# Kernel optimization log

Hardware: AMD Instinct MI355X
Metric: run time of the kernel (lower is better)

The kernel has to match this reference:

```python
import jax, jax.numpy as jnp
import numpy as np

B, S, H = 4, 1024, 1024
N, D = 16, 64  # num_heads, head_dim (key_dim = value_dim = H // N)
FF = 4096
EPS = 1e-5


def _glorot(key, shape):
    fan_in, fan_out = shape[-2], shape[-1]
    lim = np.sqrt(6.0 / (fan_in + fan_out))
    return jax.random.uniform(key, shape, jnp.float32, -lim, lim)


def setup_inputs() -> dict:
    key = jax.random.key(0)
    ks = jax.random.split(key, 32)
    inp = {
        "x": jax.random.normal(ks[0], (B, S, H), jnp.float32),
        # per-head complex Q/K projections (ComplexDense = two real Dense layers)
        "Wq_r": _glorot(ks[1], (N, H, D)), "Wq_i": _glorot(ks[2], (N, H, D)),
        "bq_r": jnp.zeros((N, D)), "bq_i": jnp.zeros((N, D)),
        "Wk_r": _glorot(ks[3], (N, H, D)), "Wk_i": _glorot(ks[4], (N, H, D)),
        "bk_r": jnp.zeros((N, D)), "bk_i": jnp.zeros((N, D)),
        # per-head real value projection
        "Wv": _glorot(ks[5], (N, H, D)), "bv": jnp.zeros((N, D)),
        # per-head positional interference weights (seq_len, key_dim)
        "pos_q_r": _glorot(ks[6], (N, S, D)), "pos_q_i": _glorot(ks[7], (N, S, D)),
        "pos_k_r": _glorot(ks[8], (N, S, D)), "pos_k_i": _glorot(ks[9], (N, S, D)),
        # multi-head output projection
        "Wo": _glorot(ks[10], (H, H)), "bo": jnp.zeros((H,)),
        # feedforward
        "W1": _glorot(ks[11], (H, FF)), "b1": jnp.zeros((FF,)),
        "W2": _glorot(ks[12], (FF, H)), "b2": jnp.zeros((H,)),
        # layer norms
        "g1": jnp.ones((H,)), "beta1": jnp.zeros((H,)),
        "g2": jnp.ones((H,)), "beta2": jnp.zeros((H,)),
    }
    return inp


def _layer_norm(x, g, b):
    mu = jnp.mean(x, axis=-1, keepdims=True)
    var = jnp.mean(jnp.square(x - mu), axis=-1, keepdims=True)
    return (x - mu) * jax.lax.rsqrt(var + EPS) * g + b


def reference(x, Wq_r, Wq_i, bq_r, bq_i, Wk_r, Wk_i, bk_r, bk_i, Wv, bv,
              pos_q_r, pos_q_i, pos_k_r, pos_k_i, Wo, bo, W1, b1, W2, b2,
              g1, beta1, g2, beta2):
    scale = 1.0 / np.sqrt(float(D))  # applied twice, as in the original
    # complex Q/K projections, all heads at once: [B,N,S,D]
    qr = jnp.einsum('bsh,nhd->bnsd', x, Wq_r) + bq_r[:, None, :]
    qi = jnp.einsum('bsh,nhd->bnsd', x, Wq_i) + bq_i[:, None, :]
    kr = jnp.einsum('bsh,nhd->bnsd', x, Wk_r) + bk_r[:, None, :]
    ki = jnp.einsum('bsh,nhd->bnsd', x, Wk_i) + bk_i[:, None, :]
    v = jnp.einsum('bsh,nhd->bnsd', x, Wv) + bv[:, None, :]
    # query scaled by 1/sqrt(D), then positional interference added (query and key)
    qr = qr * scale + pos_q_r[None]
    qi = qi * scale + pos_q_i[None]
    kr = kr + pos_k_r[None]
    ki = ki + pos_k_i[None]
    # real part of complex matmul q @ k^T (transpose_b, no conjugation), rescaled
    scores = (jnp.einsum('bnsd,bntd->bnst', qr, kr)
              - jnp.einsum('bnsd,bntd->bnst', qi, ki)) * scale
    probs = jax.nn.softmax(scores, axis=-1)  # temperature == 1.0 (use_temperature=False)
    heads = jnp.einsum('bnst,bntd->bnsd', probs, v)
    concat = heads.transpose(0, 2, 1, 3).reshape(x.shape[0], x.shape[1], N * D)
    attn_out = concat @ Wo + bo
    h1 = _layer_norm(x + attn_out, g1, beta1)
    ff = jax.nn.relu(h1 @ W1 + b1) @ W2 + b2
    return _layer_norm(h1 + ff, g2, beta2)
```

## Files before the change

### kernel.cpp

```cpp
#include <hip/hip_runtime.h>
#include <math.h>

typedef unsigned short u16;
typedef unsigned int   u32;
typedef __attribute__((ext_vector_type(8))) short short8;
typedef __attribute__((ext_vector_type(4))) float f32x4;
typedef __attribute__((ext_vector_type(4))) u16   us4;

constexpr int Bc = 4, Sc = 1024, Hc = 1024, Nc = 16, Dc = 64, FFc = 4096;

__device__ __forceinline__ u16 bfh(float v) {
  u32 u = __float_as_uint(v);
  return (u16)((u + 0x7FFFu + ((u >> 16) & 1u)) >> 16);
}
__device__ __forceinline__ void split2(float v, u16& h, u16& l) {
  h = bfh(v);
  l = bfh(v - __uint_as_float(((u32)h) << 16));
}

__device__ __forceinline__ void gl_lds16(const u16* g, u16* lds) {
  __builtin_amdgcn_global_load_lds(
      (const __attribute__((address_space(1))) void*)g,
      (__attribute__((address_space(3))) void*)lds, 16, 0, 0);
}

__device__ __forceinline__ f32x4 mfma_bf16(short8 a, short8 b, f32x4 c) {
  asm("v_mfma_f32_16x16x32_bf16 %0, %1, %2, %0" : "+v"(c) : "v"(a), "v"(b));
  return c;
}

__global__ __launch_bounds__(256)
void split_copy(const float* __restrict__ in, u16* __restrict__ oh,
                u16* __restrict__ ol, int n4) {
  int i = blockIdx.x * 256 + threadIdx.x;
  if (i >= n4) return;
  f32x4 v = ((const f32x4*)in)[i];
  us4 h4, l4;
#pragma unroll
  for (int c = 0; c < 4; ++c) { u16 h, l; split2(v[c], h, l); h4[c] = h; l4[c] = l; }
  ((us4*)oh)[i] = h4;
  ((us4*)ol)[i] = l4;
}

__global__ __launch_bounds__(256)
void transpose_split(const float* __restrict__ in, u16* __restrict__ oh,
                     u16* __restrict__ ol, int R, int C) {
  __shared__ float t[32][33];
  const int c0 = blockIdx.x * 32, r0 = blockIdx.y * 32;
  const int tx = threadIdx.x & 31, ty = threadIdx.x >> 5;
#pragma unroll
  for (int j = 0; j < 4; ++j)
    t[ty + 8 * j][tx] = in[(size_t)(r0 + ty + 8 * j) * C + c0 + tx];
  __syncthreads();
#pragma unroll
  for (int j = 0; j < 4; ++j) {
    float v = t[tx][ty + 8 * j];
    u16 h, l; split2(v, h, l);
    size_t o = (size_t)(c0 + ty + 8 * j) * R + r0 + tx;
    oh[o] = h; ol[o] = l;
  }
}

__global__ __launch_bounds__(256)
void conv_wproj(const float* __restrict__ Wqr, const float* __restrict__ Wqi,
                const float* __restrict__ Wkr, const float* __restrict__ Wki,
                const float* __restrict__ Wv,  u16* __restrict__ oh,
                u16* __restrict__ ol) {
  __shared__ float t[32][33];
  const int c0 = blockIdx.x * 32, k0 = blockIdx.y * 32;
  const int n = c0 / 320, w0 = c0 - n * 320;
  const int chunk = w0 >> 6, d0 = w0 & 63;
  const float* src; float sgn = 1.f;
  switch (chunk) {
    case 0: src = Wqr; break;
    case 1: src = Wqi; break;
    case 2: src = Wkr; break;
    case 3: src = Wki; sgn = -1.f; break;
    default: src = Wv; break;
  }
  const int tx = threadIdx.x & 31, ty = threadIdx.x >> 5;
#pragma unroll
  for (int j = 0; j < 4; ++j)
    t[ty + 8 * j][tx] = sgn * src[((size_t)n * 1024 + k0 + ty + 8 * j) * 64 + d0 + tx];
  __syncthreads();
#pragma unroll
  for (int j = 0; j < 4; ++j) {
    float v = t[tx][ty + 8 * j];
    u16 h, l; split2(v, h, l);
    size_t o = (size_t)(c0 + ty + 8 * j) * 1024 + k0 + tx;
    oh[o] = h; ol[o] = l;
  }
}

struct GemmP {
  const u16 *Ah, *Al, *Bh, *Bl;
  int N, K;
  const float* bias;
  const float* resid;
  float* outf;
  u16 *oh, *ol;
  const float *bqr, *bqi, *bkr, *bki, *bv;
  const float *pqr, *pqi, *pkr, *pki;
  u16 *qh, *ql, *kh, *kl, *vth, *vtl;
};

template<int MODE>
__global__ __launch_bounds__(256)
void mfma_gemm(GemmP p) {
  __shared__ __attribute__((aligned(16))) u16 sAh[128 * 32];
  __shared__ __attribute__((aligned(16))) u16 sAl[128 * 32];
  __shared__ __attribute__((aligned(16))) u16 sBh[128 * 32];
  __shared__ __attribute__((aligned(16))) u16 sBl[128 * 32];
  const int tid = threadIdx.x;
  const int w = tid >> 6, lane = tid & 63;
  const int wm = w >> 1, wn = w & 1;
  const int lrow = lane & 15, g = lane >> 4;
  const int bm = blockIdx.y * 128, bn = blockIdx.x * 128;
  const int K = p.K;

  const int srow = lane >> 2;
  const int sseg = (lane & 3) ^ ((lane >> 3) & 3);

  f32x4 acc[4][4];
#pragma unroll
  for (int i = 0; i < 4; ++i)
#pragma unroll
    for (int j = 0; j < 4; ++j) acc[i][j] = (f32x4){0.f, 0.f, 0.f, 0.f};

  for (int kb = 0; kb < K; kb += 32) {
#pragma unroll
    for (int i = 0; i < 2; ++i) {
      const int rowl = w * 32 + i * 16;
      const size_t ga = (size_t)(bm + rowl + srow) * K + kb + sseg * 8;
      const size_t gb = (size_t)(bn + rowl + srow) * K + kb + sseg * 8;
      const int lo = rowl * 32;
      gl_lds16(p.Ah + ga, &sAh[lo]);
      gl_lds16(p.Al + ga, &sAl[lo]);
      gl_lds16(p.Bh + gb, &sBh[lo]);
      gl_lds16(p.Bl + gb, &sBl[lo]);
    }
    __syncthreads();

    short8 ah[4], al[4], bh[4], bl[4];
    const int sw = (lrow >> 1) & 3;
#pragma unroll
    for (int mf = 0; mf < 4; ++mf) {
      int idx = (wm * 64 + mf * 16 + lrow) * 32 + ((g ^ sw) * 8);
      ah[mf] = *(const short8*)&sAh[idx];
      al[mf] = *(const short8*)&sAl[idx];
    }
#pragma unroll
    for (int nf = 0; nf < 4; ++nf) {
      int idx = (wn * 64 + nf * 16 + lrow) * 32 + ((g ^ sw) * 8);
      bh[nf] = *(const short8*)&sBh[idx];
      bl[nf] = *(const short8*)&sBl[idx];
    }
#pragma unroll
    for (int mf = 0; mf < 4; ++mf)
#pragma unroll
      for (int nf = 0; nf < 4; ++nf) {
        f32x4 a = acc[mf][nf];
        a = mfma_bf16(ah[mf], bh[nf], a);
        a = mfma_bf16(ah[mf], bl[nf], a);
        a = mfma_bf16(al[mf], bh[nf], a);
        acc[mf][nf] = a;
      }
    __syncthreads();
  }

#pragma unroll
  for (int nf = 0; nf < 4; ++nf) {
    const int c = bn + wn * 64 + nf * 16 + lrow;
    if (MODE == 0) {
      const int n = c / 320;
      const int wcol = c - n * 320;
      const int chunk = wcol >> 6, d = wcol & 63;
#pragma unroll
      for (int mf = 0; mf < 4; ++mf) {
        const int r0 = bm + wm * 64 + mf * 16 + g * 4;
        const int bb = r0 >> 10, s0 = r0 & 1023;
        const int head = bb * 16 + n;
        f32x4 a = acc[mf][nf];
        if (chunk == 4) {
          us4 hv, lv;
#pragma unroll
          for (int reg = 0; reg < 4; ++reg) {
            u16 hh, ll; split2(a[reg] + p.bv[n * 64 + d], hh, ll);
            hv[reg] = hh; lv[reg] = ll;
          }
          size_t o = ((size_t)head * 64 + d) * 1024 + s0;
          *(us4*)&p.vth[o] = hv;
          *(us4*)&p.vtl[o] = lv;
        } else {
#pragma unroll
          for (int reg = 0; reg < 4; ++reg) {
            const int s = s0 + reg;
            const size_t pidx = ((size_t)n * 1024 + s) * 64 + d;
            float val;
            u16 *dh, *dl;
            if (chunk == 0) {
              val = (a[reg] + p.bqr[n * 64 + d]) * 0.125f + p.pqr[pidx];
              dh = p.qh; dl = p.ql;
            } else if (chunk == 1) {
              val = (a[reg] + p.bqi[n * 64 + d]) * 0.125f + p.pqi[pidx];
              dh = p.qh; dl = p.ql;
            } else if (chunk == 2) {
              val = a[reg] + p.bkr[n * 64 + d] + p.pkr[pidx];
              dh = p.kh; dl = p.kl;
            } else {
              val = a[reg] - p.bki[n * 64 + d] - p.pki[pidx];
              dh = p.kh; dl = p.kl;
            }
            size_t o = ((size_t)head * 1024 + s) * 128 + (chunk & 1) * 64 + d;
            u16 hh, ll; split2(val, hh, ll);
            dh[o] = hh; dl[o] = ll;
          }
        }
      }
    } else {
      const float bb = p.bias[c];
#pragma unroll
      for (int mf = 0; mf < 4; ++mf) {
        const int r0 = bm + wm * 64 + mf * 16 + g * 4;
        f32x4 a = acc[mf][nf];
#pragma unroll
        for (int reg = 0; reg < 4; ++reg) {
          const int row = r0 + reg;
          const size_t o = (size_t)row * p.N + c;
          if (MODE == 1) {
            p.outf[o] = a[reg] + bb + p.resid[o];
          } else {
            float v = fmaxf(a[reg] + bb, 0.f);
            u16 h, l; split2(v, h, l);
            p.oh[o] = h; p.ol[o] = l;
          }
        }
      }
    }
  }
}

__global__ __launch_bounds__(256)
void attn_mfma(const u16* __restrict__ qh, const u16* __restrict__ ql,
               const u16* __restrict__ kh, const u16* __restrict__ kl,
               const u16* __restrict__ vth, const u16* __restrict__ vtl,
               u16* __restrict__ ch, u16* __restrict__ cl) {
  __shared__ __attribute__((aligned(16))) u16 ksh[64 * 128];
  __shared__ __attribute__((aligned(16))) u16 ksl[64 * 128];
  __shared__ __attribute__((aligned(16))) u16 vsh[64 * 64];
  __shared__ __attribute__((aligned(16))) u16 vsl[64 * 64];
  __shared__ __attribute__((aligned(16))) u16 ps[4][2][16 * 64];

  const int tid = threadIdx.x;
  const int w = tid >> 6, lane = tid & 63;
  const int lo16 = lane & 15, hi4 = lane >> 4;
  const int n = blockIdx.y, b = blockIdx.z;
  const int head = b * Nc + n;
  const int q0 = blockIdx.x * 64;
  const u16* qbh = qh + (size_t)head * 1024 * 128;
  const u16* qbl = ql + (size_t)head * 1024 * 128;
  const u16* kbh = kh + (size_t)head * 1024 * 128;
  const u16* kbl = kl + (size_t)head * 1024 * 128;
  const u16* vbh = vth + (size_t)head * 64 * 1024;
  const u16* vbl = vtl + (size_t)head * 64 * 1024;

  {
    const int ri = lane >> 4, slot = lane & 15;
#pragma unroll
    for (int i = 0; i < 4; ++i) {
      const int row = w * 16 + i * 4 + ri;
      const int sg = slot ^ (row & 7);
      const size_t src = (size_t)(q0 + row) * 128 + sg * 8;
      gl_lds16(qbh + src, &ksh[(w * 16 + i * 4) * 128]);
      gl_lds16(qbl + src, &ksl[(w * 16 + i * 4) * 128]);
    }
  }
  __syncthreads();
  short8 qf[2][4];
  {
    const int qrow = w * 16 + lo16;
#pragma unroll
    for (int ks = 0; ks < 4; ++ks) {
      const int addr = qrow * 128 + (((ks * 4 + hi4) ^ (qrow & 7)) * 8);
      qf[0][ks] = *(const short8*)&ksh[addr];
      qf[1][ks] = *(const short8*)&ksl[addr];
    }
  }
  __syncthreads();

  f32x4 acc_o[4];
  float m_[4], l_[4];
#pragma unroll
  for (int i = 0; i < 4; ++i) {
    acc_o[i] = (f32x4){0.f, 0.f, 0.f, 0.f};
    m_[i] = -1e30f; l_[i] = 0.f;
  }

  for (int kt = 0; kt < 16; ++kt) {
    const int k0 = kt * 64;
    {
      const int ri = lane >> 4, slot = lane & 15;
#pragma unroll
      for (int i = 0; i < 4; ++i) {
        const int row = w * 16 + i * 4 + ri;
        const int sg = slot ^ (row & 7);
        const size_t src = (size_t)(k0 + row) * 128 + sg * 8;
        gl_lds16(kbh + src, &ksh[(w * 16 + i * 4) * 128]);
        gl_lds16(kbl + src, &ksl[(w * 16 + i * 4) * 128]);
      }
      const int di = lane >> 3, vslot = lane & 7;
#pragma unroll
      for (int i = 0; i < 2; ++i) {
        const int d = w * 16 + i * 8 + di;
        const int sg = vslot ^ (d & 7);
        const size_t src = (size_t)d * 1024 + k0 + sg * 8;
        gl_lds16(vbh + src, &vsh[(w * 16 + i * 8) * 64]);
        gl_lds16(vbl + src, &vsl[(w * 16 + i * 8) * 64]);
      }
    }
    __syncthreads();

    f32x4 sc[4];
#pragma unroll
    for (int cg = 0; cg < 4; ++cg) sc[cg] = (f32x4){0.f, 0.f, 0.f, 0.f};
#pragma unroll
    for (int cg = 0; cg < 4; ++cg) {
      const int key = cg * 16 + lo16;
#pragma unroll
      for (int ks = 0; ks < 4; ++ks) {
        const int addr = key * 128 + (((ks * 4 + hi4) ^ (key & 7)) * 8);
        short8 bhf = *(const short8*)&ksh[addr];
        short8 blf = *(const short8*)&ksl[addr];
        f32x4 a = sc[cg];
        a = mfma_bf16(qf[0][ks], bhf, a);
        a = mfma_bf16(qf[0][ks], blf, a);
        a = mfma_bf16(qf[1][ks], bhf, a);
        sc[cg] = a;
      }
    }
    float pv[4][4];
#pragma unroll
    for (int reg = 0; reg < 4; ++reg) {
      float mx = fmaxf(fmaxf(sc[0][reg], sc[1][reg]),
                       fmaxf(sc[2][reg], sc[3][reg])) * 0.125f;
#pragma unroll
      for (int off = 1; off < 16; off <<= 1) mx = fmaxf(mx, __shfl_xor(mx, off));
      const float mn = fmaxf(m_[reg], mx);
      const float corr = __expf(m_[reg] - mn);
      m_[reg] = mn;
      float sum = 0.f;
#pragma unroll
      for (int cg = 0; cg < 4; ++cg) {
        float pe = __expf(sc[cg][reg] * 0.125f - mn);
        pv[cg][reg] = pe; sum += pe;
      }
#pragma unroll
      for (int off = 1; off < 16; off <<= 1) sum += __shfl_xor(sum, off);
      l_[reg] = l_[reg] * corr + sum;
#pragma unroll
      for (int cg = 0; cg < 4; ++cg) acc_o[cg][reg] *= corr;
    }
#pragma unroll
    for (int cg = 0; cg < 4; ++cg) {
      const int key = cg * 16 + lo16;
#pragma unroll
      for (int reg = 0; reg < 4; ++reg) {
        const int row = hi4 * 4 + reg;
        const int pa = row * 64 + (((key >> 3) ^ (row >> 1)) * 8) + (key & 7);
        u16 hh, ll; split2(pv[cg][reg], hh, ll);
        ps[w][0][pa] = hh;
        ps[w][1][pa] = ll;
      }
    }
    short8 pah[2], pal[2];
#pragma unroll
    for (int ks2 = 0; ks2 < 2; ++ks2) {
      const int addr = lo16 * 64 + (((ks2 * 4 + hi4) ^ (lo16 >> 1)) * 8);
      pah[ks2] = *(const short8*)&ps[w][0][addr];
      pal[ks2] = *(const short8*)&ps[w][1][addr];
    }
#pragma unroll
    for (int cg = 0; cg < 4; ++cg) {
      const int d = cg * 16 + lo16;
#pragma unroll
      for (int ks2 = 0; ks2 < 2; ++ks2) {
        const int addr = d * 64 + (((ks2 * 4 + hi4) ^ (d & 7)) * 8);
        short8 vhf = *(const short8*)&vsh[addr];
        short8 vlf = *(const short8*)&vsl[addr];
        f32x4 a = acc_o[cg];
        a = mfma_bf16(pah[ks2], vhf, a);
        a = mfma_bf16(pah[ks2], vlf, a);
        a = mfma_bf16(pal[ks2], vhf, a);
        acc_o[cg] = a;
      }
    }
    __syncthreads();
  }

  float inv[4];
#pragma unroll
  for (int reg = 0; reg < 4; ++reg) inv[reg] = 1.f / l_[reg];
#pragma unroll
  for (int cg = 0; cg < 4; ++cg) {
#pragma unroll
    for (int reg = 0; reg < 4; ++reg) {
      const int qrow = q0 + w * 16 + hi4 * 4 + reg;
      const size_t o = ((size_t)b * Sc + qrow) * 1024 + n * 64 + cg * 16 + lo16;
      u16 hh, ll; split2(acc_o[cg][reg] * inv[reg], hh, ll);
      ch[o] = hh; cl[o] = ll;
    }
  }
}

template<bool SPLIT>
__global__ __launch_bounds__(256)
void ln_kernel(const float* __restrict__ in, const float* __restrict__ gam,
               const float* __restrict__ bet, float* __restrict__ out,
               u16* __restrict__ oh, u16* __restrict__ ol) {
  const int row = blockIdx.x, t = threadIdx.x;
  f32x4 v = ((const f32x4*)(in + (size_t)row * 1024))[t];
  float s = v[0] + v[1] + v[2] + v[3];
  float q = v[0] * v[0] + v[1] * v[1] + v[2] * v[2] + v[3] * v[3];
#pragma unroll
  for (int off = 1; off < 64; off <<= 1) {
    s += __shfl_xor(s, off);
    q += __shfl_xor(q, off);
  }
  __shared__ float red[8];
  int wv = t >> 6, lnid = t & 63;
  if (lnid == 0) { red[wv] = s; red[4 + wv] = q; }
  __syncthreads();
  s = red[0] + red[1] + red[2] + red[3];
  q = red[4] + red[5] + red[6] + red[7];
  float mu = s * (1.f / 1024.f);
  float var = q * (1.f / 1024.f) - mu * mu;
  float ri = rsqrtf(var + 1e-5f);
  f32x4 g4 = ((const f32x4*)gam)[t];
  f32x4 b4 = ((const f32x4*)bet)[t];
  f32x4 o;
#pragma unroll
  for (int c = 0; c < 4; ++c) o[c] = (v[c] - mu) * ri * g4[c] + b4[c];
  ((f32x4*)(out + (size_t)row * 1024))[t] = o;
  if (SPLIT) {
    us4 h4, l4;
#pragma unroll
    for (int c = 0; c < 4; ++c) {
      u16 hh, ll; split2(o[c], hh, ll);
      h4[c] = hh; l4[c] = ll;
    }
    *(us4*)&oh[(size_t)row * 1024 + t * 4] = h4;
    *(us4*)&ol[(size_t)row * 1024 + t * 4] = l4;
  }
}

extern "C" void kernel_launch(void* const* d_in, const int* in_sizes, int n_in,
                              void* d_out, int out_size, void* d_ws, size_t ws_size,
                              hipStream_t stream) {
  const float* x    = (const float*)d_in[0];
  const float* Wq_r = (const float*)d_in[1];
  const float* Wq_i = (const float*)d_in[2];
  const float* bq_r = (const float*)d_in[3];
  const float* bq_i = (const float*)d_in[4];
  const float* Wk_r = (const float*)d_in[5];
  const float* Wk_i = (const float*)d_in[6];
  const float* bk_r = (const float*)d_in[7];
  const float* bk_i = (const float*)d_in[8];
  const float* Wv   = (const float*)d_in[9];
  const float* bv   = (const float*)d_in[10];
  const float* pq_r = (const float*)d_in[11];
  const float* pq_i = (const float*)d_in[12];
  const float* pk_r = (const float*)d_in[13];
  const float* pk_i = (const float*)d_in[14];
  const float* Wo   = (const float*)d_in[15];
  const float* bo   = (const float*)d_in[16];
  const float* W1   = (const float*)d_in[17];
  const float* b1   = (const float*)d_in[18];
  const float* W2   = (const float*)d_in[19];
  const float* b2   = (const float*)d_in[20];
  const float* g1   = (const float*)d_in[21];
  const float* be1  = (const float*)d_in[22];
  const float* g2   = (const float*)d_in[23];
  const float* be2  = (const float*)d_in[24];

  char* Wb = (char*)d_ws;
  const size_t MB = (size_t)1 << 20;
  u16* qch = (u16*)(Wb + 0 * MB);
  u16* qcl = (u16*)(Wb + 16 * MB);
  u16* kch = (u16*)(Wb + 32 * MB);
  u16* kcl = (u16*)(Wb + 48 * MB);
  u16* vth = (u16*)(Wb + 64 * MB);
  u16* vtl = (u16*)(Wb + 72 * MB);
  u16* xh  = (u16*)(Wb + 80 * MB);
  u16* xl  = (u16*)(Wb + 88 * MB);
  u16* ch  = xh; u16* cl = xl;
  u16* w2h = xh; u16* w2l = xl;
  u16* wph = (u16*)(Wb + 96 * MB);
  u16* wpl = (u16*)(Wb + 106 * MB);
  u16* w1h = (u16*)(Wb + 96 * MB);
  u16* w1l = (u16*)(Wb + 104 * MB);
  u16* woh = (u16*)(Wb + 116 * MB);
  u16* wol = (u16*)(Wb + 118 * MB);
  float* h1 = (float*)(Wb + 120 * MB);
  u16* h1h = (u16*)(Wb + 136 * MB);
  u16* h1l = (u16*)(Wb + 144 * MB);
  float* hpre = (float*)(Wb + 0 * MB);
  u16* ffh = (u16*)(Wb + 16 * MB);
  u16* ffl = (u16*)(Wb + 48 * MB);

  split_copy<<<4096, 256, 0, stream>>>(x, xh, xl, (Bc * Sc * Hc) / 4);
  conv_wproj<<<dim3(160, 32), 256, 0, stream>>>(Wq_r, Wq_i, Wk_r, Wk_i, Wv, wph, wpl);
  GemmP pp = {};
  pp.Ah = xh; pp.Al = xl; pp.Bh = wph; pp.Bl = wpl; pp.N = 5120; pp.K = 1024;
  pp.bqr = bq_r; pp.bqi = bq_i; pp.bkr = bk_r; pp.bki = bk_i; pp.bv = bv;
  pp.pqr = pq_r; pp.pqi = pq_i; pp.pkr = pk_r; pp.pki = pk_i;
  pp.qh = qch; pp.ql = qcl; pp.kh = kch; pp.kl = kcl; pp.vth = vth; pp.vtl = vtl;
  mfma_gemm<0><<<dim3(40, 32), 256, 0, stream>>>(pp);
  transpose_split<<<dim3(128, 32), 256, 0, stream>>>(W1, w1h, w1l, 1024, 4096);
  transpose_split<<<dim3(32, 32), 256, 0, stream>>>(Wo, woh, wol, 1024, 1024);
  attn_mfma<<<dim3(16, 16, 4), 256, 0, stream>>>(qch, qcl, kch, kcl, vth, vtl, ch, cl);
  GemmP po = {};
  po.Ah = ch; po.Al = cl; po.Bh = woh; po.Bl = wol; po.N = 1024; po.K = 1024;
  po.bias = bo; po.resid = x; po.outf = hpre;
  mfma_gemm<1><<<dim3(8, 32), 256, 0, stream>>>(po);
  transpose_split<<<dim3(32, 128), 256, 0, stream>>>(W2, w2h, w2l, 4096, 1024);
  ln_kernel<true><<<4096, 256, 0, stream>>>(hpre, g1, be1, h1, h1h, h1l);
  GemmP p1 = {};
  p1.Ah = h1h; p1.Al = h1l; p1.Bh = w1h; p1.Bl = w1l; p1.N = 4096; p1.K = 1024;
  p1.bias = b1; p1.oh = ffh; p1.ol = ffl;
  mfma_gemm<2><<<dim3(32, 32), 256, 0, stream>>>(p1);
  GemmP p2 = {};
  p2.Ah = ffh; p2.Al = ffl; p2.Bh = w2h; p2.Bl = w2l; p2.N = 1024; p2.K = 4096;
  p2.bias = b2; p2.resid = h1; p2.outf = hpre;
  mfma_gemm<1><<<dim3(8, 32), 256, 0, stream>>>(p2);
  ln_kernel<false><<<4096, 256, 0, stream>>>(hpre, g2, be2, (float*)d_out,
                                             nullptr, nullptr);
}
```

Baseline: 902.6 us.

## Double-buffer LDS tiles in split-bf16 MFMA GEMM to overlap loads with compute

Doubles the shared-memory staging buffers so the global-to-LDS copy of the next K slice is issued before the MFMA work on the current slice, unrolling the K loop by two. The aim is to hide global load latency that previously stalled every iteration between its load and its barrier. LDS use doubles to 64 KB per block, which may cut occupancy. The loop also assumes K is a multiple of 64.

```diff
diff --git a/kernel.cpp b/kernel.cpp
--- a/kernel.cpp
+++ b/kernel.cpp
@@ -107,10 +107,8 @@
 template<int MODE>
 __global__ __launch_bounds__(256)
 void mfma_gemm(GemmP p) {
-  __shared__ __attribute__((aligned(16))) u16 sAh[128 * 32];
-  __shared__ __attribute__((aligned(16))) u16 sAl[128 * 32];
-  __shared__ __attribute__((aligned(16))) u16 sBh[128 * 32];
-  __shared__ __attribute__((aligned(16))) u16 sBl[128 * 32];
+  __shared__ __attribute__((aligned(16))) u16 sA[2][2][128 * 32];
+  __shared__ __attribute__((aligned(16))) u16 sB[2][2][128 * 32];
   const int tid = threadIdx.x;
   const int w = tid >> 6, lane = tid & 63;
   const int wm = w >> 1, wn = w & 1;
@@ -120,6 +118,7 @@
 
   const int srow = lane >> 2;
   const int sseg = (lane & 3) ^ ((lane >> 3) & 3);
+  const int rowl0 = w * 32, rowl1 = w * 32 + 16;
 
   f32x4 acc[4][4];
 #pragma unroll
@@ -127,33 +126,35 @@
 #pragma unroll
     for (int j = 0; j < 4; ++j) acc[i][j] = (f32x4){0.f, 0.f, 0.f, 0.f};
 
-  for (int kb = 0; kb < K; kb += 32) {
-#pragma unroll
-    for (int i = 0; i < 2; ++i) {
-      const int rowl = w * 32 + i * 16;
-      const size_t ga = (size_t)(bm + rowl + srow) * K + kb + sseg * 8;
-      const size_t gb = (size_t)(bn + rowl + srow) * K + kb + sseg * 8;
-      const int lo = rowl * 32;
-      gl_lds16(p.Ah + ga, &sAh[lo]);
-      gl_lds16(p.Al + ga, &sAl[lo]);
-      gl_lds16(p.Bh + gb, &sBh[lo]);
-      gl_lds16(p.Bl + gb, &sBl[lo]);
-    }
-    __syncthreads();
-
+  auto stage = [&](int buf, int kb) {
+    const size_t ga0 = (size_t)(bm + rowl0 + srow) * K + kb + sseg * 8;
+    const size_t gb0 = (size_t)(bn + rowl0 + srow) * K + kb + sseg * 8;
+    const size_t ga1 = (size_t)(bm + rowl1 + srow) * K + kb + sseg * 8;
+    const size_t gb1 = (size_t)(bn + rowl1 + srow) * K + kb + sseg * 8;
+    gl_lds16(p.Ah + ga0, &sA[buf][0][rowl0 * 32]);
+    gl_lds16(p.Al + ga0, &sA[buf][1][rowl0 * 32]);
+    gl_lds16(p.Bh + gb0, &sB[buf][0][rowl0 * 32]);
+    gl_lds16(p.Bl + gb0, &sB[buf][1][rowl0 * 32]);
+    gl_lds16(p.Ah + ga1, &sA[buf][0][rowl1 * 32]);
+    gl_lds16(p.Al + ga1, &sA[buf][1][rowl1 * 32]);
+    gl_lds16(p.Bh + gb1, &sB[buf][0][rowl1 * 32]);
+    gl_lds16(p.Bl + gb1, &sB[buf][1][rowl1 * 32]);
+  };
+
+  const int sw = (lrow >> 1) & 3;
+  auto compute = [&](int buf) {
     short8 ah[4], al[4], bh[4], bl[4];
-    const int sw = (lrow >> 1) & 3;
 #pragma unroll
     for (int mf = 0; mf < 4; ++mf) {
       int idx = (wm * 64 + mf * 16 + lrow) * 32 + ((g ^ sw) * 8);
-      ah[mf] = *(const short8*)&sAh[idx];
-      al[mf] = *(const short8*)&sAl[idx];
+      ah[mf] = *(const short8*)&sA[buf][0][idx];
+      al[mf] = *(const short8*)&sA[buf][1][idx];
     }
 #pragma unroll
     for (int nf = 0; nf < 4; ++nf) {
       int idx = (wn * 64 + nf * 16 + lrow) * 32 + ((g ^ sw) * 8);
-      bh[nf] = *(const short8*)&sBh[idx];
-      bl[nf] = *(const short8*)&sBl[idx];
+      bh[nf] = *(const short8*)&sB[buf][0][idx];
+      bl[nf] = *(const short8*)&sB[buf][1][idx];
     }
 #pragma unroll
     for (int mf = 0; mf < 4; ++mf)
@@ -165,6 +166,16 @@
         a = mfma_bf16(al[mf], bh[nf], a);
         acc[mf][nf] = a;
       }
+  };
+
+  stage(0, 0);
+  __syncthreads();
+  for (int kb = 0; kb < K; kb += 64) {
+    stage(1, kb + 32);
+    compute(0);
+    __syncthreads();
+    if (kb + 64 < K) stage(0, kb + 64);
+    compute(1);
     __syncthreads();
   }
 
```

Result: no change. 917.6 us (+1.7%).

## Split-K the N=1024 GEMMs, fold bias/residual into LayerNorm, swizzle block order

Applied to the files above, without the earlier changes.

The output-projection and FF2 GEMMs now run with a two-way split-K (grid z=2). Each half writes raw fp32 partials to its own buffer. That doubles the block count on these narrow N=1024 GEMMs, which filled only 256 tiles before. LayerNorm is extended to sum the two partials plus bias and residual before normalising, so the GEMM epilogue no longer reads the residual. All GEMMs also remap block indices with an interleave-by-8 swizzle to change tile traversal order for cache locality. The cost is extra fp32 partial traffic (two full output-sized writes and reads) and a reshuffled workspace layout that reuses freed buffers.

```diff
diff --git a/kernel.cpp b/kernel.cpp
--- a/kernel.cpp
+++ b/kernel.cpp
@@ -94,10 +94,10 @@
 
 struct GemmP {
   const u16 *Ah, *Al, *Bh, *Bl;
-  int N, K;
+  int N, K, lda;
   const float* bias;
-  const float* resid;
   float* outf;
+  float* outf1;
   u16 *oh, *ol;
   const float *bqr, *bqi, *bkr, *bki, *bv;
   const float *pqr, *pqi, *pkr, *pki;
@@ -107,19 +107,23 @@
 template<int MODE>
 __global__ __launch_bounds__(256)
 void mfma_gemm(GemmP p) {
-  __shared__ __attribute__((aligned(16))) u16 sAh[128 * 32];
-  __shared__ __attribute__((aligned(16))) u16 sAl[128 * 32];
-  __shared__ __attribute__((aligned(16))) u16 sBh[128 * 32];
-  __shared__ __attribute__((aligned(16))) u16 sBl[128 * 32];
+  __shared__ __attribute__((aligned(16))) u16 sA[2][128 * 32];
+  __shared__ __attribute__((aligned(16))) u16 sB[2][128 * 32];
   const int tid = threadIdx.x;
   const int w = tid >> 6, lane = tid & 63;
   const int wm = w >> 1, wn = w & 1;
   const int lrow = lane & 15, g = lane >> 4;
-  const int bm = blockIdx.y * 128, bn = blockIdx.x * 128;
-  const int K = p.K;
+  const int gx = gridDim.x;
+  const int id = blockIdx.y * gx + blockIdx.x;
+  const int qq = (gx * gridDim.y) >> 3;
+  const int sid = (id & 7) * qq + (id >> 3);
+  const int bn = (sid % gx) * 128, bm = (sid / gx) * 128;
+  const int K = p.K, lda = p.lda;
+  const int koff = blockIdx.z * K;
 
   const int srow = lane >> 2;
   const int sseg = (lane & 3) ^ ((lane >> 3) & 3);
+  const int rowl0 = w * 32, rowl1 = w * 32 + 16;
 
   f32x4 acc[4][4];
 #pragma unroll
@@ -127,33 +131,34 @@
 #pragma unroll
     for (int j = 0; j < 4; ++j) acc[i][j] = (f32x4){0.f, 0.f, 0.f, 0.f};
 
+  const int sw = (lrow >> 1) & 3;
   for (int kb = 0; kb < K; kb += 32) {
-#pragma unroll
-    for (int i = 0; i < 2; ++i) {
-      const int rowl = w * 32 + i * 16;
-      const size_t ga = (size_t)(bm + rowl + srow) * K + kb + sseg * 8;
-      const size_t gb = (size_t)(bn + rowl + srow) * K + kb + sseg * 8;
-      const int lo = rowl * 32;
-      gl_lds16(p.Ah + ga, &sAh[lo]);
-      gl_lds16(p.Al + ga, &sAl[lo]);
-      gl_lds16(p.Bh + gb, &sBh[lo]);
-      gl_lds16(p.Bl + gb, &sBl[lo]);
-    }
+    const size_t ga0 = (size_t)(bm + rowl0 + srow) * lda + koff + kb + sseg * 8;
+    const size_t gb0 = (size_t)(bn + rowl0 + srow) * lda + koff + kb + sseg * 8;
+    const size_t ga1 = (size_t)(bm + rowl1 + srow) * lda + koff + kb + sseg * 8;
+    const size_t gb1 = (size_t)(bn + rowl1 + srow) * lda + koff + kb + sseg * 8;
+    gl_lds16(p.Ah + ga0, &sA[0][rowl0 * 32]);
+    gl_lds16(p.Al + ga0, &sA[1][rowl0 * 32]);
+    gl_lds16(p.Bh + gb0, &sB[0][rowl0 * 32]);
+    gl_lds16(p.Bl + gb0, &sB[1][rowl0 * 32]);
+    gl_lds16(p.Ah + ga1, &sA[0][rowl1 * 32]);
+    gl_lds16(p.Al + ga1, &sA[1][rowl1 * 32]);
+    gl_lds16(p.Bh + gb1, &sB[0][rowl1 * 32]);
+    gl_lds16(p.Bl + gb1, &sB[1][rowl1 * 32]);
     __syncthreads();
 
     short8 ah[4], al[4], bh[4], bl[4];
-    const int sw = (lrow >> 1) & 3;
 #pragma unroll
     for (int mf = 0; mf < 4; ++mf) {
       int idx = (wm * 64 + mf * 16 + lrow) * 32 + ((g ^ sw) * 8);
-      ah[mf] = *(const short8*)&sAh[idx];
-      al[mf] = *(const short8*)&sAl[idx];
+      ah[mf] = *(const short8*)&sA[0][idx];
+      al[mf] = *(const short8*)&sA[1][idx];
     }
 #pragma unroll
     for (int nf = 0; nf < 4; ++nf) {
       int idx = (wn * 64 + nf * 16 + lrow) * 32 + ((g ^ sw) * 8);
-      bh[nf] = *(const short8*)&sBh[idx];
-      bl[nf] = *(const short8*)&sBl[idx];
+      bh[nf] = *(const short8*)&sB[0][idx];
+      bl[nf] = *(const short8*)&sB[1][idx];
     }
 #pragma unroll
     for (int mf = 0; mf < 4; ++mf)
@@ -217,23 +222,28 @@
           }
         }
       }
-    } else {
-      const float bb = p.bias[c];
+    } else if (MODE == 1) {
+      float* outp = blockIdx.z ? p.outf1 : p.outf;
 #pragma unroll
       for (int mf = 0; mf < 4; ++mf) {
         const int r0 = bm + wm * 64 + mf * 16 + g * 4;
         f32x4 a = acc[mf][nf];
 #pragma unroll
+        for (int reg = 0; reg < 4; ++reg)
+          outp[(size_t)(r0 + reg) * p.N + c] = a[reg];
+      }
+    } else {
+      const float bb = p.bias[c];
+#pragma unroll
+      for (int mf = 0; mf < 4; ++mf) {
+        const int r0 = bm + wm * 64 + mf * 16 + g * 4;
+        f32x4 a = acc[mf][nf];
+#pragma unroll
         for (int reg = 0; reg < 4; ++reg) {
-          const int row = r0 + reg;
-          const size_t o = (size_t)row * p.N + c;
-          if (MODE == 1) {
-            p.outf[o] = a[reg] + bb + p.resid[o];
-          } else {
-            float v = fmaxf(a[reg] + bb, 0.f);
-            u16 h, l; split2(v, h, l);
-            p.oh[o] = h; p.ol[o] = l;
-          }
+          const size_t o = (size_t)(r0 + reg) * p.N + c;
+          float v = fmaxf(a[reg] + bb, 0.f);
+          u16 h, l; split2(v, h, l);
+          p.oh[o] = h; p.ol[o] = l;
         }
       }
     }
@@ -414,11 +424,19 @@
 
 template<bool SPLIT>
 __global__ __launch_bounds__(256)
-void ln_kernel(const float* __restrict__ in, const float* __restrict__ gam,
-               const float* __restrict__ bet, float* __restrict__ out,
-               u16* __restrict__ oh, u16* __restrict__ ol) {
+void ln_fuse(const float* __restrict__ P0, const float* __restrict__ P1,
+             const float* __restrict__ resid, const float* __restrict__ bias,
+             const float* __restrict__ gam, const float* __restrict__ bet,
+             float* __restrict__ out, u16* __restrict__ oh,
+             u16* __restrict__ ol) {
   const int row = blockIdx.x, t = threadIdx.x;
-  f32x4 v = ((const f32x4*)(in + (size_t)row * 1024))[t];
+  const size_t base = (size_t)row * 1024;
+  f32x4 v = ((const f32x4*)(P0 + base))[t];
+  f32x4 p1 = ((const f32x4*)(P1 + base))[t];
+  f32x4 rr = ((const f32x4*)(resid + base))[t];
+  f32x4 bb = ((const f32x4*)bias)[t];
+#pragma unroll
+  for (int c = 0; c < 4; ++c) v[c] += p1[c] + rr[c] + bb[c];
   float s = v[0] + v[1] + v[2] + v[3];
   float q = v[0] * v[0] + v[1] * v[1] + v[2] * v[2] + v[3] * v[3];
 #pragma unroll
@@ -440,7 +458,7 @@
   f32x4 o;
 #pragma unroll
   for (int c = 0; c < 4; ++c) o[c] = (v[c] - mu) * ri * g4[c] + b4[c];
-  ((f32x4*)(out + (size_t)row * 1024))[t] = o;
+  ((f32x4*)(out + base))[t] = o;
   if (SPLIT) {
     us4 h4, l4;
 #pragma unroll
@@ -448,8 +466,8 @@
       u16 hh, ll; split2(o[c], hh, ll);
       h4[c] = hh; l4[c] = ll;
     }
-    *(us4*)&oh[(size_t)row * 1024 + t * 4] = h4;
-    *(us4*)&ol[(size_t)row * 1024 + t * 4] = l4;
+    *(us4*)&oh[base + t * 4] = h4;
+    *(us4*)&ol[base + t * 4] = l4;
   }
 }
 
@@ -498,19 +516,23 @@
   u16* wpl = (u16*)(Wb + 106 * MB);
   u16* w1h = (u16*)(Wb + 96 * MB);
   u16* w1l = (u16*)(Wb + 104 * MB);
-  u16* woh = (u16*)(Wb + 116 * MB);
-  u16* wol = (u16*)(Wb + 118 * MB);
+  u16* woh = (u16*)(Wb + 112 * MB);
+  u16* wol = (u16*)(Wb + 114 * MB);
   float* h1 = (float*)(Wb + 120 * MB);
   u16* h1h = (u16*)(Wb + 136 * MB);
   u16* h1l = (u16*)(Wb + 144 * MB);
-  float* hpre = (float*)(Wb + 0 * MB);
-  u16* ffh = (u16*)(Wb + 16 * MB);
-  u16* ffl = (u16*)(Wb + 48 * MB);
+  float* P0 = (float*)(Wb + 0 * MB);
+  float* P1 = (float*)(Wb + 16 * MB);
+  u16* ffh = (u16*)(Wb + 0 * MB);
+  u16* ffl = (u16*)(Wb + 32 * MB);
+  float* Q0 = (float*)(Wb + 64 * MB);
+  float* Q1 = (float*)(Wb + 96 * MB);
 
   split_copy<<<4096, 256, 0, stream>>>(x, xh, xl, (Bc * Sc * Hc) / 4);
   conv_wproj<<<dim3(160, 32), 256, 0, stream>>>(Wq_r, Wq_i, Wk_r, Wk_i, Wv, wph, wpl);
   GemmP pp = {};
-  pp.Ah = xh; pp.Al = xl; pp.Bh = wph; pp.Bl = wpl; pp.N = 5120; pp.K = 1024;
+  pp.Ah = xh; pp.Al = xl; pp.Bh = wph; pp.Bl = wpl;
+  pp.N = 5120; pp.K = 1024; pp.lda = 1024;
   pp.bqr = bq_r; pp.bqi = bq_i; pp.bkr = bk_r; pp.bki = bk_i; pp.bv = bv;
   pp.pqr = pq_r; pp.pqi = pq_i; pp.pkr = pk_r; pp.pki = pk_i;
   pp.qh = qch; pp.ql = qcl; pp.kh = kch; pp.kl = kcl; pp.vth = vth; pp.vtl = vtl;
@@ -519,19 +541,22 @@
   transpose_split<<<dim3(32, 32), 256, 0, stream>>>(Wo, woh, wol, 1024, 1024);
   attn_mfma<<<dim3(16, 16, 4), 256, 0, stream>>>(qch, qcl, kch, kcl, vth, vtl, ch, cl);
   GemmP po = {};
-  po.Ah = ch; po.Al = cl; po.Bh = woh; po.Bl = wol; po.N = 1024; po.K = 1024;
-  po.bias = bo; po.resid = x; po.outf = hpre;
-  mfma_gemm<1><<<dim3(8, 32), 256, 0, stream>>>(po);
+  po.Ah = ch; po.Al = cl; po.Bh = woh; po.Bl = wol;
+  po.N = 1024; po.K = 512; po.lda = 1024;
+  po.outf = P0; po.outf1 = P1;
+  mfma_gemm<1><<<dim3(8, 32, 2), 256, 0, stream>>>(po);
   transpose_split<<<dim3(32, 128), 256, 0, stream>>>(W2, w2h, w2l, 4096, 1024);
-  ln_kernel<true><<<4096, 256, 0, stream>>>(hpre, g1, be1, h1, h1h, h1l);
+  ln_fuse<true><<<4096, 256, 0, stream>>>(P0, P1, x, bo, g1, be1, h1, h1h, h1l);
   GemmP p1 = {};
-  p1.Ah = h1h; p1.Al = h1l; p1.Bh = w1h; p1.Bl = w1l; p1.N = 4096; p1.K = 1024;
+  p1.Ah = h1h; p1.Al = h1l; p1.Bh = w1h; p1.Bl = w1l;
+  p1.N = 4096; p1.K = 1024; p1.lda = 1024;
   p1.bias = b1; p1.oh = ffh; p1.ol = ffl;
   mfma_gemm<2><<<dim3(32, 32), 256, 0, stream>>>(p1);
   GemmP p2 = {};
-  p2.Ah = ffh; p2.Al = ffl; p2.Bh = w2h; p2.Bl = w2l; p2.N = 1024; p2.K = 4096;
-  p2.bias = b2; p2.resid = h1; p2.outf = hpre;
-  mfma_gemm<1><<<dim3(8, 32), 256, 0, stream>>>(p2);
-  ln_kernel<false><<<4096, 256, 0, stream>>>(hpre, g2, be2, (float*)d_out,
-                                             nullptr, nullptr);
-}
+  p2.Ah = ffh; p2.Al = ffl; p2.Bh = w2h; p2.Bl = w2l;
+  p2.N = 1024; p2.K = 2048; p2.lda = 4096;
+  p2.outf = Q0; p2.outf1 = Q1;
+  mfma_gemm<1><<<dim3(8, 32, 2), 256, 0, stream>>>(p2);
+  ln_fuse<false><<<4096, 256, 0, stream>>>(Q0, Q1, h1, b2, g2, be2,
+                                           (float*)d_out, nullptr, nullptr);
+}
```

Measured after the change: 825.1 us. 1.09x faster.
